# Kernel tuning notes

Measured on AMD Instinct MI355X. Metric: run time of the kernel, lower is better.

Reference implementation:

```python
import jax, jax.numpy as jnp
import numpy as np
import math

B, C, HH, WW = 4, 256, 64, 64
NUM_HEADS = 4
GROUPS = 8
EPS = 1e-5


def setup_inputs() -> dict:
    key = jax.random.key(0)
    k1, k2, k3 = jax.random.split(key, 3)
    x = jax.random.normal(k1, (B, C, HH, WW), dtype=jnp.float32)
    gn_w = jnp.ones((C,), dtype=jnp.float32)
    gn_b = jnp.zeros((C,), dtype=jnp.float32)
    qkv_w = jax.random.normal(k2, (3 * C, C), dtype=jnp.float32) * (1.0 / math.sqrt(C))
    qkv_b = jnp.zeros((3 * C,), dtype=jnp.float32)
    proj_w = jax.random.normal(k3, (C, C), dtype=jnp.float32) * (1.0 / math.sqrt(C))
    proj_b = jnp.zeros((C,), dtype=jnp.float32)
    return {"x": x, "gn_w": gn_w, "gn_b": gn_b, "qkv_w": qkv_w,
            "qkv_b": qkv_b, "proj_w": proj_w, "proj_b": proj_b}


def reference(x, gn_w, gn_b, qkv_w, qkv_b, proj_w, proj_b):
    b, c, h, w = x.shape
    nh = NUM_HEADS
    d = c // nh          # head dim = 64
    s = h * w            # sequence length = 4096

    # GroupNorm(8, c): normalize over (c//G, h, w) per group, biased variance
    xg = x.reshape(b, GROUPS, c // GROUPS, h, w)
    mu = xg.mean(axis=(2, 3, 4), keepdims=True)
    var = xg.var(axis=(2, 3, 4), keepdims=True)
    xn = ((xg - mu) * jax.lax.rsqrt(var + EPS)).reshape(b, c, h, w)
    xn = xn * gn_w[None, :, None, None] + gn_b[None, :, None, None]

    # 1x1 conv QKV == channel-wise matmul
    qkv = jnp.einsum('oc,bchw->bohw', qkv_w, xn) + qkv_b[None, :, None, None]
    qkv = qkv.reshape(b, 3, nh, d, s)
    q = jnp.transpose(qkv[:, 0], (0, 1, 3, 2))  # [b, nh, s, d]
    k = jnp.transpose(qkv[:, 1], (0, 1, 3, 2))
    v = jnp.transpose(qkv[:, 2], (0, 1, 3, 2))

    scale = 1.0 / math.sqrt(d)
    attn = jnp.einsum('bhqd,bhkd->bhqk', q, k) * scale  # [b, nh, s, s]
    attn = jax.nn.softmax(attn, axis=-1)
    out = jnp.einsum('bhqk,bhkd->bhqd', attn, v)        # [b, nh, s, d]

    out = jnp.transpose(out, (0, 1, 3, 2)).reshape(b, c, h, w)
    out = jnp.einsum('oc,bchw->bohw', proj_w, out) + proj_b[None, :, None, None]
    return out + x
```

## Files before the change

### kernel.cpp

```cpp
#include <hip/hip_runtime.h>
#include <hip/hip_bf16.h>

#define B_ 4
#define C_ 256
#define S_ 4096
#define NH_ 4
#define HD_ 64
#define LOG2E 1.4426950408889634f
#define QSC 0.18033688011112042f

typedef __attribute__((ext_vector_type(8))) short short8;
typedef __attribute__((ext_vector_type(4))) short short4v;
typedef __attribute__((ext_vector_type(4))) float f32x4;
typedef __attribute__((ext_vector_type(16))) float f32x16;
typedef __attribute__((ext_vector_type(4))) unsigned uint4v;

static __device__ __forceinline__ short f2bf(float f) {
  unsigned u = __builtin_bit_cast(unsigned, f);
  u += 0x7fffu + ((u >> 16) & 1u);
  return (short)(u >> 16);
}
static __device__ __forceinline__ float bf2f(short h) {
  unsigned u = ((unsigned)(unsigned short)h) << 16;
  return __builtin_bit_cast(float, u);
}

#if __has_builtin(__builtin_amdgcn_exp2f)
#define EXP2(x) __builtin_amdgcn_exp2f(x)
#else
#define EXP2(x) exp2f(x)
#endif

static __device__ __forceinline__ unsigned pkbf(float a, float b) {
  unsigned r;
  asm("v_cvt_pk_bf16_f32 %0, %1, %2" : "=v"(r) : "v"(a), "v"(b));
  return r;
}
static __device__ __forceinline__ void pl32swap(unsigned& a, unsigned& b) {
  asm volatile("v_permlane32_swap_b32 %0, %1" : "+v"(a), "+v"(b));
}
static __device__ __forceinline__ void gl_lds16(const short* g, char* l) {
  __builtin_amdgcn_global_load_lds(
      (const __attribute__((address_space(1))) void*)g,
      (__attribute__((address_space(3))) void*)l, 16, 0, 0);
}

__global__ __launch_bounds__(256) void k_pre(const float* __restrict__ x,
                                             const float* __restrict__ wq,
                                             const float* __restrict__ wp,
                                             float* __restrict__ part,
                                             short* __restrict__ oq,
                                             short* __restrict__ op) {
  int t = threadIdx.x;
  const float* p = x + (size_t)blockIdx.x * 16384;
  float s = 0.f, ss = 0.f;
  const float4* p4 = reinterpret_cast<const float4*>(p);
  for (int i = t; i < 4096; i += 256) {
    float4 v = p4[i];
    s += v.x + v.y + v.z + v.w;
    ss += v.x * v.x + v.y * v.y + v.z * v.z + v.w * v.w;
  }
  for (int m = 1; m < 64; m <<= 1) {
    s += __shfl_xor(s, m, 64);
    ss += __shfl_xor(ss, m, 64);
  }
  __shared__ float rs[4], rss[4];
  int w = t >> 6;
  if ((t & 63) == 0) { rs[w] = s; rss[w] = ss; }
  {
    int i = (blockIdx.x * 256 + t) * 4;
    const int n1 = 768 * 256;
    float sc = 1.f;
    const float* src;
    short* dst;
    if (i < n1) {
      src = wq + i; dst = oq + i;
      if (i < 256 * 256) sc = QSC;
    } else {
      src = wp + (i - n1); dst = op + (i - n1);
    }
    float4 v = *reinterpret_cast<const float4*>(src);
    short4v o;
    o[0] = f2bf(v.x * sc); o[1] = f2bf(v.y * sc);
    o[2] = f2bf(v.z * sc); o[3] = f2bf(v.w * sc);
    *reinterpret_cast<short4v*>(dst) = o;
  }
  __syncthreads();
  if (t == 0) {
    part[2 * blockIdx.x] = rs[0] + rs[1] + rs[2] + rs[3];
    part[2 * blockIdx.x + 1] = rss[0] + rss[1] + rss[2] + rss[3];
  }
}

__global__ __launch_bounds__(256) void k_gn_apply(const float* __restrict__ x,
                                                  const float* __restrict__ gw,
                                                  const float* __restrict__ gb,
                                                  const float* __restrict__ part,
                                                  short* __restrict__ xnt) {
  int st = blockIdx.x;
  int ct = blockIdx.y;
  int b = blockIdx.z;
  int t = threadIdx.x;
  __shared__ short T[64 * 72];
  __shared__ float smu[2], sri[2];
  int c0 = ct * 64, s0 = st * 64;
  if (t < 2) {
    int g = (c0 >> 5) + t;
    int base = b * 64 + g * 8;
    float s = 0.f, ss = 0.f;
    for (int j = 0; j < 8; j++) {
      s += part[2 * (base + j)];
      ss += part[2 * (base + j) + 1];
    }
    float inv = 1.f / (32.f * S_);
    float mu = s * inv;
    float var = ss * inv - mu * mu;
    smu[t] = mu;
    sri[t] = rsqrtf(var + 1e-5f);
  }
  __syncthreads();
  int r4 = t >> 4;
  int f4 = t & 15;
  for (int p = 0; p < 4; p++) {
    int r = p * 16 + r4;
    int c = c0 + r;
    int gl = r >> 5;
    float mu = smu[gl];
    float ri = sri[gl];
    float A = gw[c] * ri;
    float Bb = gb[c] - mu * A;
    float4 v = *reinterpret_cast<const float4*>(x + ((size_t)(b * C_ + c)) * S_ + s0 + f4 * 4);
    int sb = f4 * 4;
    T[(sb + 0) * 72 + r] = f2bf(v.x * A + Bb);
    T[(sb + 1) * 72 + r] = f2bf(v.y * A + Bb);
    T[(sb + 2) * 72 + r] = f2bf(v.z * A + Bb);
    T[(sb + 3) * 72 + r] = f2bf(v.w * A + Bb);
  }
  __syncthreads();
  for (int it = 0; it < 2; it++) {
    int cch = t + it * 256;
    int sl = cch >> 3, c8 = cch & 7;
    short8 v = *reinterpret_cast<short8*>(&T[sl * 72 + c8 * 8]);
    *reinterpret_cast<short8*>(xnt + ((size_t)(b * S_ + s0 + sl)) * C_ + c0 + c8 * 8) = v;
  }
}

template <int MODE, int NSP>
__global__ __launch_bounds__(256) void k_gemm(const short* __restrict__ Wbf,
                                              const short* __restrict__ Xt,
                                              const float* __restrict__ bias,
                                              const float* __restrict__ xres,
                                              short* __restrict__ q_sd,
                                              short* __restrict__ k_sd,
                                              short* __restrict__ v_ds,
                                              long op_stride,
                                              const float* __restrict__ lbufg,
                                              float* __restrict__ outp) {
  int tn = blockIdx.x;
  int tm = blockIdx.y;
  int b = blockIdx.z;
  int t = threadIdx.x;
  __shared__ short lds[4 * 64 * 72];
  char* glds = (char*)lds;
  short* Blp = lds + 4096;
  int w = t >> 6, lane = t & 63;
  int wr = w >> 1, wc = w & 1;
  int l15 = lane & 15, l4 = lane >> 4;
  int wbg = __builtin_amdgcn_readfirstlane(w) << 10;

  f32x4 acc[4][4];
  for (int m = 0; m < 4; m++)
    for (int n = 0; n < 4; n++)
      for (int j = 0; j < 4; j++) acc[m][n][j] = 0.f;

  const short* Arow = Wbf + (size_t)(tm * 128) * 256;
  const short* Brow = Xt + ((size_t)b * S_ + tn * 128) * 256;

  int r0 = t >> 2, c40 = t & 3;
  int sw0 = (c40 ^ ((r0 >> 1) & 3)) * 8;
  int r1 = (t + 256) >> 2;
  int sw1 = (c40 ^ ((r1 >> 1) & 3)) * 8;

  if (MODE == 0) {
    gl_lds16(Arow + (size_t)r0 * 256 + sw0, glds + wbg);
    gl_lds16(Arow + (size_t)r1 * 256 + sw1, glds + 4096 + wbg);
    gl_lds16(Brow + (size_t)r0 * 256 + sw0, glds + 8192 + wbg);
    gl_lds16(Brow + (size_t)r1 * 256 + sw1, glds + 12288 + wbg);
    asm volatile("s_waitcnt vmcnt(0)" ::: "memory");
    __builtin_amdgcn_s_barrier();
    asm volatile("" ::: "memory");
    for (int step = 0; step < 8; step++) {
      char* cb = glds + ((step & 1) << 14);
      if (step + 1 < 8) {
        char* nb = glds + (((step + 1) & 1) << 14);
        int kk = (step + 1) * 32;
        gl_lds16(Arow + (size_t)r0 * 256 + kk + sw0, nb + wbg);
        gl_lds16(Arow + (size_t)r1 * 256 + kk + sw1, nb + 4096 + wbg);
        gl_lds16(Brow + (size_t)r0 * 256 + kk + sw0, nb + 8192 + wbg);
        gl_lds16(Brow + (size_t)r1 * 256 + kk + sw1, nb + 12288 + wbg);
      }
      short8 af[4], bf[4];
      for (int mt = 0; mt < 4; mt++) {
        int row = wr * 64 + mt * 16 + l15;
        af[mt] = *reinterpret_cast<short8*>(cb + row * 64 + ((l4 ^ ((row >> 1) & 3)) << 4));
      }
      for (int nt = 0; nt < 4; nt++) {
        int row = wc * 64 + nt * 16 + l15;
        bf[nt] = *reinterpret_cast<short8*>(cb + 8192 + row * 64 + ((l4 ^ ((row >> 1) & 3)) << 4));
      }
      for (int mt = 0; mt < 4; mt++)
        for (int nt = 0; nt < 4; nt++)
          acc[mt][nt] =
              __builtin_amdgcn_mfma_f32_16x16x32_bf16(af[mt], bf[nt], acc[mt][nt], 0, 0, 0);
      if (step + 1 < 8) {
        asm volatile("s_waitcnt vmcnt(0)" ::: "memory");
        __builtin_amdgcn_s_barrier();
        asm volatile("" ::: "memory");
      }
    }
  } else {
    for (int kk = 0; kk < 256; kk += 32) {
      __syncthreads();
      gl_lds16(Arow + (size_t)r0 * 256 + kk + sw0, glds + wbg);
      gl_lds16(Arow + (size_t)r1 * 256 + kk + sw1, glds + 4096 + wbg);
      for (int i = 0; i < 2; i++) {
        int cch = t + i * 256;
        int r = cch >> 2, c4 = cch & 3;
        int c = kk + c4 * 8;
        int bh2 = b * 4 + (c >> 6);
        int d = c & 63;
        int s_glob = tn * 128 + r;
        size_t ro = ((size_t)bh2 * S_ + s_glob) * HD_ + d;
        float a8[8] = {0.f, 0.f, 0.f, 0.f, 0.f, 0.f, 0.f, 0.f};
        float l = 0.f;
#pragma unroll
        for (int i2 = 0; i2 < NSP; i2++) {
          short8 pv = *reinterpret_cast<const short8*>(Xt + (size_t)i2 * op_stride + ro);
#pragma unroll
          for (int j = 0; j < 8; j++) a8[j] += bf2f(pv[j]);
          l += lbufg[(size_t)(i2 * 16 + bh2) * S_ + s_glob];
        }
        float inv = 1.f / l;
        short8 vbv;
#pragma unroll
        for (int j = 0; j < 8; j++) vbv[j] = f2bf(a8[j] * inv);
        *reinterpret_cast<short8*>(&Blp[r * 40 + c4 * 8]) = vbv;
      }
      asm volatile("s_waitcnt vmcnt(0)" ::: "memory");
      __syncthreads();

      short8 af[4], bf[4];
      for (int mt = 0; mt < 4; mt++) {
        int row = wr * 64 + mt * 16 + l15;
        af[mt] = *reinterpret_cast<short8*>(glds + row * 64 + ((l4 ^ ((row >> 1) & 3)) << 4));
      }
      for (int nt = 0; nt < 4; nt++) {
        int row = wc * 64 + nt * 16 + l15;
        bf[nt] = *reinterpret_cast<short8*>(&Blp[row * 40 + l4 * 8]);
      }
      for (int mt = 0; mt < 4; mt++)
        for (int nt = 0; nt < 4; nt++)
          acc[mt][nt] =
              __builtin_amdgcn_mfma_f32_16x16x32_bf16(af[mt], bf[nt], acc[mt][nt], 0, 0, 0);
    }
  }
  __syncthreads();

  if (MODE == 0) {
    int o_base = tm * 128 + wr * 64;
    int tt = o_base >> 8;
    int h = (o_base >> 6) & 3;
    int s_base = tn * 128 + wc * 64;
    int bh = b * NH_ + h;
    if (tt == 2) {
      for (int mt = 0; mt < 4; mt++)
        for (int nt = 0; nt < 4; nt++)
          for (int i = 0; i < 4; i++) {
            int o = o_base + mt * 16 + l4 * 4 + i;
            int dd = o & 63;
            int s = s_base + nt * 16 + l15;
            float val = acc[mt][nt][i] + bias[o];
            v_ds[((size_t)bh * HD_ + dd) * S_ + s] = f2bf(val);
          }
    } else {
      float bsc = (tt == 0) ? QSC : 1.f;
      short* T = lds + w * (64 * 72);
      for (int mt = 0; mt < 4; mt++)
        for (int nt = 0; nt < 4; nt++)
          for (int i = 0; i < 4; i++) {
            int o = o_base + mt * 16 + l4 * 4 + i;
            int dd = mt * 16 + l4 * 4 + i;
            int sl = nt * 16 + l15;
            float val = acc[mt][nt][i] + bias[o] * bsc;
            T[sl * 72 + dd] = f2bf(val);
          }
      short* dst = (tt == 0) ? q_sd : k_sd;
      for (int it = 0; it < 8; it++) {
        int cch = lane + it * 64;
        int sl = cch >> 3, c8 = cch & 7;
        short8 v = *reinterpret_cast<short8*>(&T[sl * 72 + c8 * 8]);
        *reinterpret_cast<short8*>(dst + ((size_t)bh * S_ + s_base + sl) * HD_ + c8 * 8) = v;
      }
    }
  } else {
    for (int mt = 0; mt < 4; mt++) {
      int o = tm * 128 + wr * 64 + mt * 16 + l4 * 4;
      for (int nt = 0; nt < 4; nt++) {
        int s = tn * 128 + wc * 64 + nt * 16 + l15;
        for (int i = 0; i < 4; i++) {
          size_t off = ((size_t)(b * C_ + o + i)) * S_ + s;
          outp[off] = acc[mt][nt][i] + bias[o + i] + xres[off];
        }
      }
    }
  }
}

__global__ __launch_bounds__(256, 2) void k_attn(const short* __restrict__ q_sd,
                                                 const short* __restrict__ k_sd,
                                                 const short* __restrict__ v_ds,
                                                 short* __restrict__ op_base,
                                                 long op_stride,
                                                 float* __restrict__ lbuf,
                                                 int ntile) {
  int bid = blockIdx.x;
  int qt = bid >> 5;
  int bh = (bid >> 1) & 15;
  int sk = bid & 1;
  int t = threadIdx.x, w = t >> 6, lane = t & 63;
  int l31 = lane & 31, hi = lane >> 5, hi8 = hi * 8;
  int qb = qt * 256 + w * 64;

  __shared__ char smem[49152];

  int wb = __builtin_amdgcn_readfirstlane(w) << 10;

  int r8 = t >> 3, s8 = t & 7;
  int sw8 = (s8 ^ (r8 & 7)) * 8;
  const short* kb = k_sd + ((size_t)bh * S_ + (size_t)sk * ntile * 64) * HD_;
  const short* vbg = v_ds + (size_t)bh * HD_ * S_ + sk * ntile * 64;
  int koff0 = r8 * 64 + sw8;
  int koff1 = koff0 + 32 * 64;
  size_t voff0 = (size_t)r8 * S_ + sw8;
  size_t voff1 = voff0 + (size_t)32 * S_;

#define STAGE(bsel, ti)                                                        \
  do {                                                                         \
    const short* kt_ = kb + (size_t)(ti) * (64 * HD_);                         \
    const short* vt_ = vbg + (ti) * 64;                                        \
    char* lb_ = smem + ((bsel) << 14) + wb;                                    \
    gl_lds16(kt_ + koff0, lb_);                                                \
    gl_lds16(kt_ + koff1, lb_ + 4096);                                         \
    gl_lds16(vt_ + voff0, lb_ + 8192);                                         \
    gl_lds16(vt_ + voff1, lb_ + 12288);                                        \
  } while (0)

  const short* qpA = q_sd + ((size_t)bh * S_ + qb + l31) * HD_ + hi8;
  short8 qfA[4], qfB[4];
#pragma unroll
  for (int sl = 0; sl < 4; sl++) {
    qfA[sl] = *reinterpret_cast<const short8*>(qpA + sl * 16);
    qfB[sl] = *reinterpret_cast<const short8*>(qpA + 32 * HD_ + sl * 16);
  }

  int x7 = l31 & 7;
  int rb0 = l31 * 128;

  f32x16 OA0, OA1, OB0, OB1;
#pragma unroll
  for (int r = 0; r < 16; r++) { OA0[r] = 0.f; OA1[r] = 0.f; OB0[r] = 0.f; OB1[r] = 0.f; }
  float lA = 0.f, lB = 0.f;

  STAGE(0, 0);
  if (ntile > 1) STAGE(1, 1);
  asm volatile("s_waitcnt vmcnt(4)" ::: "memory");
  __builtin_amdgcn_s_barrier();
  asm volatile("" ::: "memory");

#define MKPA2(pa0, pa1, s)                                                     \
  do {                                                                         \
    unsigned c0 = pkbf(s[0], s[1]), c1 = pkbf(s[2], s[3]);                     \
    unsigned c2 = pkbf(s[4], s[5]), c3 = pkbf(s[6], s[7]);                     \
    pl32swap(c0, c2); pl32swap(c1, c3);                                        \
    uint4v u0; u0[0] = c0; u0[1] = c1; u0[2] = c2; u0[3] = c3;                 \
    pa0 = __builtin_bit_cast(short8, u0);                                      \
    unsigned c4 = pkbf(s[8], s[9]), c5 = pkbf(s[10], s[11]);                   \
    unsigned c6 = pkbf(s[12], s[13]), c7 = pkbf(s[14], s[15]);                 \
    pl32swap(c4, c6); pl32swap(c5, c7);                                        \
    uint4v u1; u1[0] = c4; u1[1] = c5; u1[2] = c6; u1[3] = c7;                 \
    pa1 = __builtin_bit_cast(short8, u1);                                      \
  } while (0)

  int cs = 0;
  for (int it = 0; it < ntile; it++) {
    char* cur = smem + (cs << 14);
    int ns = (cs == 2) ? 0 : cs + 1;
    int ps = (cs == 0) ? 2 : cs - 1;
    if (it + 2 < ntile) STAGE(ps, it + 2);

    f32x16 sA0, sB0;
#pragma unroll
    for (int r = 0; r < 16; r++) { sA0[r] = 0.f; sB0[r] = 0.f; }
    __builtin_amdgcn_s_setprio(1);
#pragma unroll
    for (int sl = 0; sl < 4; sl++) {
      int so = ((sl * 2 + hi) ^ x7) << 4;
      short8 kf0 = *reinterpret_cast<short8*>(cur + rb0 + so);
      sA0 = __builtin_amdgcn_mfma_f32_32x32x16_bf16(kf0, qfA[sl], sA0, 0, 0, 0);
      sB0 = __builtin_amdgcn_mfma_f32_32x32x16_bf16(kf0, qfB[sl], sB0, 0, 0, 0);
    }

    f32x16 sA1, sB1;
#pragma unroll
    for (int r = 0; r < 16; r++) { sA1[r] = 0.f; sB1[r] = 0.f; }
#pragma unroll
    for (int sl = 0; sl < 4; sl++) {
      int so = ((sl * 2 + hi) ^ x7) << 4;
      short8 kf1 = *reinterpret_cast<short8*>(cur + 4096 + rb0 + so);
      sA1 = __builtin_amdgcn_mfma_f32_32x32x16_bf16(kf1, qfA[sl], sA1, 0, 0, 0);
      sB1 = __builtin_amdgcn_mfma_f32_32x32x16_bf16(kf1, qfB[sl], sB1, 0, 0, 0);
#pragma unroll
      for (int j = 0; j < 4; j++) {
        sA0[sl * 4 + j] = EXP2(sA0[sl * 4 + j]);
        sB0[sl * 4 + j] = EXP2(sB0[sl * 4 + j]);
      }
    }
    __builtin_amdgcn_s_setprio(0);

    {
      float a0 = 0.f, a1 = 0.f, a2 = 0.f, a3 = 0.f;
      float b0 = 0.f, b1 = 0.f, b2 = 0.f, b3 = 0.f;
#pragma unroll
      for (int r = 0; r < 16; r += 4) {
        a0 += sA0[r]; a1 += sA0[r + 1]; a2 += sA0[r + 2]; a3 += sA0[r + 3];
        b0 += sB0[r]; b1 += sB0[r + 1]; b2 += sB0[r + 2]; b3 += sB0[r + 3];
      }
      lA += (a0 + a1) + (a2 + a3);
      lB += (b0 + b1) + (b2 + b3);
    }
    short8 paA0, paA1, paB0, paB1;
    MKPA2(paA0, paA1, sA0);
    MKPA2(paB0, paB1, sB0);

    __builtin_amdgcn_s_setprio(1);
#pragma unroll
    for (int ks = 0; ks < 2; ks++) {
      int so = ((ks * 2 + hi) ^ x7) << 4;
      short8 vf0 = *reinterpret_cast<short8*>(cur + 8192 + rb0 + so);
      short8 vf1 = *reinterpret_cast<short8*>(cur + 12288 + rb0 + so);
      short8 pA = ks ? paA1 : paA0;
      short8 pB = ks ? paB1 : paB0;
      OA0 = __builtin_amdgcn_mfma_f32_32x32x16_bf16(vf0, pA, OA0, 0, 0, 0);
      OB0 = __builtin_amdgcn_mfma_f32_32x32x16_bf16(vf0, pB, OB0, 0, 0, 0);
      OA1 = __builtin_amdgcn_mfma_f32_32x32x16_bf16(vf1, pA, OA1, 0, 0, 0);
      OB1 = __builtin_amdgcn_mfma_f32_32x32x16_bf16(vf1, pB, OB1, 0, 0, 0);
#pragma unroll
      for (int j = 0; j < 8; j++) {
        sA1[ks * 8 + j] = EXP2(sA1[ks * 8 + j]);
        sB1[ks * 8 + j] = EXP2(sB1[ks * 8 + j]);
      }
    }
    __builtin_amdgcn_s_setprio(0);

    {
      float a0 = 0.f, a1 = 0.f, a2 = 0.f, a3 = 0.f;
      float b0 = 0.f, b1 = 0.f, b2 = 0.f, b3 = 0.f;
#pragma unroll
      for (int r = 0; r < 16; r += 4) {
        a0 += sA1[r]; a1 += sA1[r + 1]; a2 += sA1[r + 2]; a3 += sA1[r + 3];
        b0 += sB1[r]; b1 += sB1[r + 1]; b2 += sB1[r + 2]; b3 += sB1[r + 3];
      }
      lA += (a0 + a1) + (a2 + a3);
      lB += (b0 + b1) + (b2 + b3);
    }
    short8 paA2, paA3, paB2, paB3;
    MKPA2(paA2, paA3, sA1);
    MKPA2(paB2, paB3, sB1);

    __builtin_amdgcn_s_setprio(1);
#pragma unroll
    for (int ks = 2; ks < 4; ks++) {
      int so = ((ks * 2 + hi) ^ x7) << 4;
      short8 vf0 = *reinterpret_cast<short8*>(cur + 8192 + rb0 + so);
      short8 vf1 = *reinterpret_cast<short8*>(cur + 12288 + rb0 + so);
      short8 pA = (ks == 2) ? paA2 : paA3;
      short8 pB = (ks == 2) ? paB2 : paB3;
      OA0 = __builtin_amdgcn_mfma_f32_32x32x16_bf16(vf0, pA, OA0, 0, 0, 0);
      OB0 = __builtin_amdgcn_mfma_f32_32x32x16_bf16(vf0, pB, OB0, 0, 0, 0);
      OA1 = __builtin_amdgcn_mfma_f32_32x32x16_bf16(vf1, pA, OA1, 0, 0, 0);
      OB1 = __builtin_amdgcn_mfma_f32_32x32x16_bf16(vf1, pB, OB1, 0, 0, 0);
    }
    __builtin_amdgcn_s_setprio(0);

    if (it + 1 < ntile) {
      if (it + 2 < ntile)
        asm volatile("s_waitcnt vmcnt(4)" ::: "memory");
      else
        asm volatile("s_waitcnt vmcnt(0)" ::: "memory");
      __builtin_amdgcn_s_barrier();
      asm volatile("" ::: "memory");
    }
    cs = ns;
  }

  lA += __shfl_xor(lA, 32, 64);
  lB += __shfl_xor(lB, 32, 64);
  short* optrA = op_base + (size_t)sk * op_stride + ((size_t)bh * S_ + qb + l31) * HD_;
  short* optrB = optrA + 32 * HD_;
#pragma unroll
  for (int qd = 0; qd < 4; qd++) {
    short4v a0, a1, b0v, b1v;
#pragma unroll
    for (int i = 0; i < 4; i++) {
      a0[i] = f2bf(OA0[qd * 4 + i]);
      a1[i] = f2bf(OA1[qd * 4 + i]);
      b0v[i] = f2bf(OB0[qd * 4 + i]);
      b1v[i] = f2bf(OB1[qd * 4 + i]);
    }
    int d0 = qd * 8 + hi * 4;
    *reinterpret_cast<short4v*>(optrA + d0) = a0;
    *reinterpret_cast<short4v*>(optrA + 32 + d0) = a1;
    *reinterpret_cast<short4v*>(optrB + d0) = b0v;
    *reinterpret_cast<short4v*>(optrB + 32 + d0) = b1v;
  }
  if (hi == 0) {
    lbuf[(size_t)(sk * 16 + bh) * S_ + qb + l31] = lA;
    lbuf[(size_t)(sk * 16 + bh) * S_ + qb + 32 + l31] = lB;
  }
#undef STAGE
#undef MKPA2
}

extern "C" void kernel_launch(void* const* d_in, const int* in_sizes, int n_in,
                              void* d_out, int out_size, void* d_ws, size_t ws_size,
                              hipStream_t stream) {
  const float* x      = (const float*)d_in[0];
  const float* gn_w   = (const float*)d_in[1];
  const float* gn_b   = (const float*)d_in[2];
  const float* qkv_w  = (const float*)d_in[3];
  const float* qkv_b  = (const float*)d_in[4];
  const float* proj_w = (const float*)d_in[5];
  const float* proj_b = (const float*)d_in[6];
  char* ws = (char*)d_ws;
  float* part  = (float*)(ws + 2048);
  short* wqkv  = (short*)(ws + 4096);
  short* wproj = (short*)(ws + 397312);
  short* xnt   = (short*)(ws + 528384);
  short* q_sd  = (short*)(ws + 8916992);
  short* k_sd  = (short*)(ws + 17305600);
  short* v_ds  = (short*)(ws + 25694208);
  short* op_base = xnt;
  long op_stride = (42471424 - 528384) / 2;
  float* lbuf  = (float*)(ws + 50860032);
  float* outp  = (float*)d_out;

  k_pre<<<256, 256, 0, stream>>>(x, qkv_w, proj_w, part, wqkv, wproj);
  k_gn_apply<<<dim3(64, 4, 4), 256, 0, stream>>>(x, gn_w, gn_b, part, xnt);
  k_gemm<0, 0><<<dim3(32, 6, 4), 256, 0, stream>>>(wqkv, xnt, qkv_b, nullptr, q_sd, k_sd, v_ds,
                                                   0, nullptr, nullptr);
  k_attn<<<512, 256, 0, stream>>>(q_sd, k_sd, v_ds, op_base, op_stride, lbuf, 32);
  k_gemm<1, 2><<<dim3(32, 2, 4), 256, 0, stream>>>(wproj, op_base, proj_b, x, nullptr, nullptr,
                                                   nullptr, op_stride, lbuf, outp);
}
```

Measured before the change: 125.2 us.

## Double-buffer merge GEMM operands and compute softmax row sums with MFMA

The output-projection GEMM mode (merging split-K attention partials) now uses ping-pong LDS buffers for both the weight tile and the merged activation tile. The next K-step's loads and merge run before the current step's MFMAs, with one barrier per step instead of two. In the attention kernel, the per-lane VALU reduction of exp values into row sums is replaced by extra MFMAs against a one-hot bf16 selector matrix, which also removes the final cross-lane shuffle. Costs: four extra MFMAs per half-tile, an extra f32x16 accumulator, and row sums now taken from bf16-rounded probabilities rather than fp32.

```diff
diff --git a/kernel.cpp b/kernel.cpp
--- a/kernel.cpp
+++ b/kernel.cpp
@@ -162,7 +162,6 @@
   int t = threadIdx.x;
   __shared__ short lds[4 * 64 * 72];
   char* glds = (char*)lds;
-  short* Blp = lds + 4096;
   int w = t >> 6, lane = t & 63;
   int wr = w >> 1, wc = w & 1;
   int l15 = lane & 15, l4 = lane >> 4;
@@ -219,50 +218,65 @@
       }
     }
   } else {
-    for (int kk = 0; kk < 256; kk += 32) {
-      __syncthreads();
-      gl_lds16(Arow + (size_t)r0 * 256 + kk + sw0, glds + wbg);
-      gl_lds16(Arow + (size_t)r1 * 256 + kk + sw1, glds + 4096 + wbg);
-      for (int i = 0; i < 2; i++) {
-        int cch = t + i * 256;
-        int r = cch >> 2, c4 = cch & 3;
-        int c = kk + c4 * 8;
-        int bh2 = b * 4 + (c >> 6);
-        int d = c & 63;
-        int s_glob = tn * 128 + r;
-        size_t ro = ((size_t)bh2 * S_ + s_glob) * HD_ + d;
-        float a8[8] = {0.f, 0.f, 0.f, 0.f, 0.f, 0.f, 0.f, 0.f};
-        float l = 0.f;
-#pragma unroll
-        for (int i2 = 0; i2 < NSP; i2++) {
-          short8 pv = *reinterpret_cast<const short8*>(Xt + (size_t)i2 * op_stride + ro);
-#pragma unroll
-          for (int j = 0; j < 8; j++) a8[j] += bf2f(pv[j]);
-          l += lbufg[(size_t)(i2 * 16 + bh2) * S_ + s_glob];
-        }
-        float inv = 1.f / l;
-        short8 vbv;
-#pragma unroll
-        for (int j = 0; j < 8; j++) vbv[j] = f2bf(a8[j] * inv);
-        *reinterpret_cast<short8*>(&Blp[r * 40 + c4 * 8]) = vbv;
-      }
-      asm volatile("s_waitcnt vmcnt(0)" ::: "memory");
-      __syncthreads();
-
+    short* Blp0 = lds + 8192;
+    short* Blp1 = lds + 8192 + 5120;
+#define MERGE_B(kk_, dstB)                                                     \
+    do {                                                                       \
+      for (int i = 0; i < 2; i++) {                                            \
+        int cch = t + i * 256;                                                 \
+        int r = cch >> 2, c4 = cch & 3;                                        \
+        int c = (kk_) + c4 * 8;                                                \
+        int bh2 = b * 4 + (c >> 6);                                            \
+        int d = c & 63;                                                        \
+        int s_glob = tn * 128 + r;                                             \
+        size_t ro = ((size_t)bh2 * S_ + s_glob) * HD_ + d;                     \
+        float a8[8] = {0.f, 0.f, 0.f, 0.f, 0.f, 0.f, 0.f, 0.f};                \
+        float l = 0.f;                                                         \
+        _Pragma("unroll") for (int i2 = 0; i2 < NSP; i2++) {                   \
+          short8 pv = *reinterpret_cast<const short8*>(                        \
+              Xt + (size_t)i2 * op_stride + ro);                               \
+          _Pragma("unroll") for (int j = 0; j < 8; j++) a8[j] += bf2f(pv[j]);  \
+          l += lbufg[(size_t)(i2 * 16 + bh2) * S_ + s_glob];                   \
+        }                                                                      \
+        float inv = 1.f / l;                                                   \
+        short8 vbv;                                                            \
+        _Pragma("unroll") for (int j = 0; j < 8; j++)                          \
+            vbv[j] = f2bf(a8[j] * inv);                                        \
+        *reinterpret_cast<short8*>(&(dstB)[r * 40 + c4 * 8]) = vbv;            \
+      }                                                                        \
+    } while (0)
+
+    gl_lds16(Arow + (size_t)r0 * 256 + sw0, glds + wbg);
+    gl_lds16(Arow + (size_t)r1 * 256 + sw1, glds + 4096 + wbg);
+    MERGE_B(0, Blp0);
+    __syncthreads();
+    for (int step = 0; step < 8; step++) {
+      char* cbA = glds + ((step & 1) ? 8192 : 0);
+      short* cbB = (step & 1) ? Blp1 : Blp0;
+      if (step + 1 < 8) {
+        char* nbA = glds + (((step + 1) & 1) ? 8192 : 0);
+        short* nbB = ((step + 1) & 1) ? Blp1 : Blp0;
+        int kk = (step + 1) * 32;
+        gl_lds16(Arow + (size_t)r0 * 256 + kk + sw0, nbA + wbg);
+        gl_lds16(Arow + (size_t)r1 * 256 + kk + sw1, nbA + 4096 + wbg);
+        MERGE_B(kk, nbB);
+      }
       short8 af[4], bf[4];
       for (int mt = 0; mt < 4; mt++) {
         int row = wr * 64 + mt * 16 + l15;
-        af[mt] = *reinterpret_cast<short8*>(glds + row * 64 + ((l4 ^ ((row >> 1) & 3)) << 4));
+        af[mt] = *reinterpret_cast<short8*>(cbA + row * 64 + ((l4 ^ ((row >> 1) & 3)) << 4));
       }
       for (int nt = 0; nt < 4; nt++) {
         int row = wc * 64 + nt * 16 + l15;
-        bf[nt] = *reinterpret_cast<short8*>(&Blp[row * 40 + l4 * 8]);
+        bf[nt] = *reinterpret_cast<short8*>(&cbB[row * 40 + l4 * 8]);
       }
       for (int mt = 0; mt < 4; mt++)
         for (int nt = 0; nt < 4; nt++)
           acc[mt][nt] =
               __builtin_amdgcn_mfma_f32_16x16x32_bf16(af[mt], bf[nt], acc[mt][nt], 0, 0, 0);
-    }
+      if (step + 1 < 8) __syncthreads();
+    }
+#undef MERGE_B
   }
   __syncthreads();
 
@@ -363,13 +377,22 @@
     qfB[sl] = *reinterpret_cast<const short8*>(qpA + 32 * HD_ + sl * 16);
   }
 
+  const short one_bf = (short)0x3F80;
+  short8 eA, eB;
+#pragma unroll
+  for (int j = 0; j < 8; j++) {
+    eA[j] = (l31 == 0) ? one_bf : (short)0;
+    eB[j] = (l31 == 1) ? one_bf : (short)0;
+  }
+
   int x7 = l31 & 7;
   int rb0 = l31 * 128;
 
-  f32x16 OA0, OA1, OB0, OB1;
-#pragma unroll
-  for (int r = 0; r < 16; r++) { OA0[r] = 0.f; OA1[r] = 0.f; OB0[r] = 0.f; OB1[r] = 0.f; }
-  float lA = 0.f, lB = 0.f;
+  f32x16 OA0, OA1, OB0, OB1, lacc;
+#pragma unroll
+  for (int r = 0; r < 16; r++) {
+    OA0[r] = 0.f; OA1[r] = 0.f; OB0[r] = 0.f; OB1[r] = 0.f; lacc[r] = 0.f;
+  }
 
   STAGE(0, 0);
   if (ntile > 1) STAGE(1, 1);
@@ -427,20 +450,13 @@
     }
     __builtin_amdgcn_s_setprio(0);
 
-    {
-      float a0 = 0.f, a1 = 0.f, a2 = 0.f, a3 = 0.f;
-      float b0 = 0.f, b1 = 0.f, b2 = 0.f, b3 = 0.f;
-#pragma unroll
-      for (int r = 0; r < 16; r += 4) {
-        a0 += sA0[r]; a1 += sA0[r + 1]; a2 += sA0[r + 2]; a3 += sA0[r + 3];
-        b0 += sB0[r]; b1 += sB0[r + 1]; b2 += sB0[r + 2]; b3 += sB0[r + 3];
-      }
-      lA += (a0 + a1) + (a2 + a3);
-      lB += (b0 + b1) + (b2 + b3);
-    }
     short8 paA0, paA1, paB0, paB1;
     MKPA2(paA0, paA1, sA0);
     MKPA2(paB0, paB1, sB0);
+    lacc = __builtin_amdgcn_mfma_f32_32x32x16_bf16(eA, paA0, lacc, 0, 0, 0);
+    lacc = __builtin_amdgcn_mfma_f32_32x32x16_bf16(eA, paA1, lacc, 0, 0, 0);
+    lacc = __builtin_amdgcn_mfma_f32_32x32x16_bf16(eB, paB0, lacc, 0, 0, 0);
+    lacc = __builtin_amdgcn_mfma_f32_32x32x16_bf16(eB, paB1, lacc, 0, 0, 0);
 
     __builtin_amdgcn_s_setprio(1);
 #pragma unroll
@@ -462,20 +478,13 @@
     }
     __builtin_amdgcn_s_setprio(0);
 
-    {
-      float a0 = 0.f, a1 = 0.f, a2 = 0.f, a3 = 0.f;
-      float b0 = 0.f, b1 = 0.f, b2 = 0.f, b3 = 0.f;
-#pragma unroll
-      for (int r = 0; r < 16; r += 4) {
-        a0 += sA1[r]; a1 += sA1[r + 1]; a2 += sA1[r + 2]; a3 += sA1[r + 3];
-        b0 += sB1[r]; b1 += sB1[r + 1]; b2 += sB1[r + 2]; b3 += sB1[r + 3];
-      }
-      lA += (a0 + a1) + (a2 + a3);
-      lB += (b0 + b1) + (b2 + b3);
-    }
     short8 paA2, paA3, paB2, paB3;
     MKPA2(paA2, paA3, sA1);
     MKPA2(paB2, paB3, sB1);
+    lacc = __builtin_amdgcn_mfma_f32_32x32x16_bf16(eA, paA2, lacc, 0, 0, 0);
+    lacc = __builtin_amdgcn_mfma_f32_32x32x16_bf16(eA, paA3, lacc, 0, 0, 0);
+    lacc = __builtin_amdgcn_mfma_f32_32x32x16_bf16(eB, paB2, lacc, 0, 0, 0);
+    lacc = __builtin_amdgcn_mfma_f32_32x32x16_bf16(eB, paB3, lacc, 0, 0, 0);
 
     __builtin_amdgcn_s_setprio(1);
 #pragma unroll
@@ -503,8 +512,6 @@
     cs = ns;
   }
 
-  lA += __shfl_xor(lA, 32, 64);
-  lB += __shfl_xor(lB, 32, 64);
   short* optrA = op_base + (size_t)sk * op_stride + ((size_t)bh * S_ + qb + l31) * HD_;
   short* optrB = optrA + 32 * HD_;
 #pragma unroll
@@ -524,8 +531,8 @@
     *reinterpret_cast<short4v*>(optrB + 32 + d0) = b1v;
   }
   if (hi == 0) {
-    lbuf[(size_t)(sk * 16 + bh) * S_ + qb + l31] = lA;
-    lbuf[(size_t)(sk * 16 + bh) * S_ + qb + 32 + l31] = lB;
+    lbuf[(size_t)(sk * 16 + bh) * S_ + qb + l31] = lacc[0];
+    lbuf[(size_t)(sk * 16 + bh) * S_ + qb + 32 + l31] = lacc[1];
   }
 #undef STAGE
 #undef MKPA2
```

Result: no change. 122.9 us (-1.8%).
